# Kernel optimization log

Measured on AMD Instinct MI355X. Metric: run time of the kernel, lower is better.

## Reference

```python
import jax, jax.numpy as jnp
import numpy as np

B, S, E, H = 4, 2048, 1024, 16
D = E // H  # head_dim


def setup_inputs() -> dict:
    key = jax.random.key(0)
    ks = jax.random.split(key, 7)
    scale = 1.0 / np.sqrt(E)
    return {
        "query": jax.random.normal(ks[0], (B, S, E), dtype=jnp.float32),
        "key": jax.random.normal(ks[1], (B, S, E), dtype=jnp.float32),
        "value": jax.random.normal(ks[2], (B, S, E), dtype=jnp.float32),
        "Wq": jax.random.normal(ks[3], (E, E), dtype=jnp.float32) * scale,
        "Wk": jax.random.normal(ks[4], (E, E), dtype=jnp.float32) * scale,
        "Wv": jax.random.normal(ks[5], (E, E), dtype=jnp.float32) * scale,
        "Wo": jax.random.normal(ks[6], (E, E), dtype=jnp.float32) * scale,
    }


def reference(query, key, value, Wq, Wk, Wv, Wo):
    b, s, e = query.shape
    sm_scale = (e // H) ** -0.5
    # TTLinear: x @ W.T; reshape to [b, h, s, d]
    q = (query @ Wq.T).reshape(b, s, H, D).transpose(0, 2, 1, 3)
    k = (key @ Wk.T).reshape(b, s, H, D).transpose(0, 2, 1, 3)
    v = (value @ Wv.T).reshape(b, s, H, D).transpose(0, 2, 1, 3)
    scores = jnp.einsum("bhqd,bhkd->bhqk", q, k) * sm_scale  # [b,h,s,s]
    attn = jax.nn.softmax(scores, axis=-1)
    out = jnp.einsum("bhqk,bhkd->bhqd", attn, v)
    out = out.transpose(0, 2, 1, 3).reshape(b, s, e)
    # dropout is identity in eval mode
    return out @ Wo.T
```

## Files before the change

kernel.cpp:

```cpp
#include <hip/hip_runtime.h>
#include <hip/hip_bf16.h>

#define BB 4
#define SS 2048
#define EE 1024
#define HH 16
#define DD 64
#define MM (BB*SS)

using f16x8 = __attribute__((ext_vector_type(8))) _Float16;
using f16x4 = __attribute__((ext_vector_type(4))) _Float16;
using f32x4 = __attribute__((ext_vector_type(4))) float;
using f32x16 = __attribute__((ext_vector_type(16))) float;

typedef __attribute__((address_space(3))) void       as3_void;
typedef const __attribute__((address_space(1))) void as1_cvoid;

__device__ __forceinline__ void async16(void* lds, const void* g) {
    __builtin_amdgcn_global_load_lds((as1_cvoid*)g, (as3_void*)lds, 16, 0, 0);
}

__device__ __forceinline__ f16x8 cvt8(const float* src) {
    const float4 v0 = *(const float4*)src;
    const float4 v1 = *(const float4*)(src + 4);
    f16x8 h;
    h[0] = (_Float16)v0.x; h[1] = (_Float16)v0.y;
    h[2] = (_Float16)v0.z; h[3] = (_Float16)v0.w;
    h[4] = (_Float16)v1.x; h[5] = (_Float16)v1.y;
    h[6] = (_Float16)v1.z; h[7] = (_Float16)v1.w;
    return h;
}

__global__ __launch_bounds__(256) void cvt_all(const float* __restrict__ q,
                                               const float* __restrict__ k,
                                               const float* __restrict__ v,
                                               const float* __restrict__ w0,
                                               const float* __restrict__ w1,
                                               const float* __restrict__ w2,
                                               const float* __restrict__ w3,
                                               _Float16* __restrict__ dq,
                                               _Float16* __restrict__ dk,
                                               _Float16* __restrict__ dv,
                                               _Float16* __restrict__ wf,
                                               int aN8, int wN8) {
    int seg = blockIdx.y;
    int i = blockIdx.x * 256 + threadIdx.x;
    const float* s; _Float16* d; int n8;
    if (seg < 3) {
        s = seg == 0 ? q : seg == 1 ? k : v;
        d = seg == 0 ? dq : seg == 1 ? dk : dv;
        n8 = aN8;
    } else {
        int t = seg - 3;
        s = t == 0 ? w0 : t == 1 ? w1 : t == 2 ? w2 : w3;
        d = wf + (size_t)t * EE * EE;
        n8 = wN8;
    }
    if (i < n8) ((f16x8*)d)[i] = cvt8(s + (size_t)i * 8);
}

__device__ __forceinline__ void swizzle512(int fid, int& m0, int& n0) {
    int xcd  = fid & 7;
    int s    = fid >> 3;
    int band = xcd + 8 * (s >> 5);
    int w    = s & 31;
    m0 = (band * 4 + (w & 3)) * 128;
    n0 = (w >> 2) * 128;
}

__global__ __launch_bounds__(256) void gemm_qkv(const _Float16* __restrict__ A0,
                                                const _Float16* __restrict__ A1,
                                                const _Float16* __restrict__ A2,
                                                const _Float16* __restrict__ W,
                                                _Float16* __restrict__ Cb,
                                                int M, int N, int K) {
    constexpr int BM = 128, BN = 128, BK = 64;
    __shared__ alignas(16) _Float16 As[2][BM * 32];
    __shared__ alignas(16) _Float16 Bs[2][BN * 32];

    const int tid  = threadIdx.x;
    const int lane = tid & 63;
    const int wave = tid >> 6;
    const int wm   = (wave >> 1) * 64;
    const int wn   = (wave & 1) * 64;
    const int quad = lane >> 4;
    const int c    = lane & 15;
    int m0, n0;
    swizzle512(blockIdx.x, m0, n0);
    const int z = blockIdx.y;

    const _Float16* A  = z == 0 ? A0 : z == 1 ? A1 : A2;
    const _Float16* Bw = W + (size_t)z * EE * EE;
    _Float16* C = Cb + (size_t)z * MM * EE;
    const float osc = (z == 0) ? 0.18033688f : 1.0f;

    f32x4 acc[4][4] = {};

    for (int k0 = 0; k0 < K; k0 += BK) {
#pragma unroll
        for (int p = 0; p < 4; ++p) {
            int half = p >> 1;
            int remb = (p & 1) * 256 + wave * 64;
            int rem  = remb + lane;
            int row  = rem >> 2, kc = (rem & 3) * 8;
            async16(&As[half][remb * 8], A  + (size_t)(m0 + row) * K + k0 + half * 32 + kc);
            async16(&Bs[half][remb * 8], Bw + (size_t)(n0 + row) * K + k0 + half * 32 + kc);
        }
        __syncthreads();

#pragma unroll
        for (int ks = 0; ks < 2; ++ks) {
            f16x8 af[4], bf[4];
#pragma unroll
            for (int i = 0; i < 4; ++i)
                af[i] = *(const f16x8*)&As[ks][(wm + i * 16 + c) * 32 + quad * 8];
#pragma unroll
            for (int j = 0; j < 4; ++j)
                bf[j] = *(const f16x8*)&Bs[ks][(wn + j * 16 + c) * 32 + quad * 8];
#pragma unroll
            for (int i = 0; i < 4; ++i)
#pragma unroll
                for (int j = 0; j < 4; ++j)
                    acc[i][j] = __builtin_amdgcn_mfma_f32_16x16x32_f16(af[i], bf[j], acc[i][j], 0, 0, 0);
        }
        __syncthreads();
    }

    if (z == 2) {
#pragma unroll
        for (int i = 0; i < 4; ++i)
#pragma unroll
            for (int j = 0; j < 4; ++j) {
                int col  = n0 + wn + j * 16 + c;
                int rowb = m0 + wm + i * 16 + quad * 4;
                int bq = rowb >> 11, sI = rowb & 2047;
                f16x4 ov;
#pragma unroll
                for (int r = 0; r < 4; ++r) ov[r] = (_Float16)acc[i][j][r];
                *(f16x4*)&C[(((size_t)bq * HH + (col >> 6)) * DD + (col & 63)) * SS + sI] = ov;
            }
    } else {
#pragma unroll
        for (int i = 0; i < 4; ++i)
#pragma unroll
            for (int j = 0; j < 4; ++j)
#pragma unroll
                for (int r = 0; r < 4; ++r) {
                    int row = m0 + wm + i * 16 + quad * 4 + r;
                    int col = n0 + wn + j * 16 + c;
                    C[(size_t)row * N + col] = (_Float16)(acc[i][j][r] * osc);
                }
    }
}

__global__ __launch_bounds__(256) void gemm_wo(const _Float16* __restrict__ A,
                                               const _Float16* __restrict__ Bw,
                                               float* __restrict__ C,
                                               int M, int N, int K) {
    constexpr int BM = 128, BN = 128, BK = 64;
    __shared__ alignas(16) _Float16 As[2][BM * 32];
    __shared__ alignas(16) _Float16 Bs[2][BN * 32];

    const int tid  = threadIdx.x;
    const int lane = tid & 63;
    const int wave = tid >> 6;
    const int wm   = (wave >> 1) * 64;
    const int wn   = (wave & 1) * 64;
    const int quad = lane >> 4;
    const int c    = lane & 15;
    int m0, n0;
    swizzle512(blockIdx.x, m0, n0);

    f32x4 acc[4][4] = {};

    for (int k0 = 0; k0 < K; k0 += BK) {
#pragma unroll
        for (int p = 0; p < 4; ++p) {
            int half = p >> 1;
            int remb = (p & 1) * 256 + wave * 64;
            int rem  = remb + lane;
            int row  = rem >> 2, kc = (rem & 3) * 8;
            async16(&As[half][remb * 8], A  + (size_t)(m0 + row) * K + k0 + half * 32 + kc);
            async16(&Bs[half][remb * 8], Bw + (size_t)(n0 + row) * K + k0 + half * 32 + kc);
        }
        __syncthreads();

#pragma unroll
        for (int ks = 0; ks < 2; ++ks) {
            f16x8 af[4], bf[4];
#pragma unroll
            for (int i = 0; i < 4; ++i)
                af[i] = *(const f16x8*)&As[ks][(wm + i * 16 + c) * 32 + quad * 8];
#pragma unroll
            for (int j = 0; j < 4; ++j)
                bf[j] = *(const f16x8*)&Bs[ks][(wn + j * 16 + c) * 32 + quad * 8];
#pragma unroll
            for (int i = 0; i < 4; ++i)
#pragma unroll
                for (int j = 0; j < 4; ++j)
                    acc[i][j] = __builtin_amdgcn_mfma_f32_16x16x32_f16(af[i], bf[j], acc[i][j], 0, 0, 0);
        }
        __syncthreads();
    }

#pragma unroll
    for (int i = 0; i < 4; ++i)
#pragma unroll
        for (int j = 0; j < 4; ++j)
#pragma unroll
            for (int r = 0; r < 4; ++r) {
                int row = m0 + wm + i * 16 + quad * 4 + r;
                int col = n0 + wn + j * 16 + c;
                C[(size_t)row * N + col] = acc[i][j][r];
            }
}

__global__ __launch_bounds__(256, 4) void attn_kernel(const _Float16* __restrict__ Q,
                                                      const _Float16* __restrict__ K,
                                                      const _Float16* __restrict__ Vt,
                                                      _Float16* __restrict__ O) {
    constexpr int NT = SS / 64;
    __shared__ alignas(16) _Float16 Ks[2][8 * 512];
    __shared__ alignas(16) _Float16 Vs[2][8 * 512];

    const int tid  = threadIdx.x;
    const int lane = tid & 63;
    const int wave = tid >> 6;
    const int l31  = lane & 31;
    const int hl   = lane >> 5;
    const int bh   = blockIdx.x;
    const int b    = bh >> 4, h = bh & 15;
    const int q0   = blockIdx.y * 128;

    const _Float16* Qg  = Q  + (size_t)(b * SS + q0) * EE + h * DD;
    const _Float16* Kg  = K  + (size_t)(b * SS) * EE + h * DD;
    const _Float16* Vtg = Vt + (size_t)bh * DD * SS;

    f16x8 qf[4];
#pragma unroll
    for (int ks = 0; ks < 4; ++ks)
        qf[ks] = *(const f16x8*)(Qg + (size_t)(wave * 32 + l31) * EE + ks * 16 + hl * 8);

    const _Float16* kp[2];
    const _Float16* vp[2];
#pragma unroll
    for (int p = 0; p < 2; ++p) {
        int f = wave * 2 + p;
        int kvt = f >> 2, ksk = f & 3;
        kp[p] = Kg + (size_t)(kvt * 32 + l31) * EE + ksk * 16 + hl * 8;
        int ksv = f >> 1, dt = f & 1;
        vp[p] = Vtg + (size_t)(dt * 32 + l31) * SS + ksv * 16 + hl * 8;
    }

#pragma unroll
    for (int p = 0; p < 2; ++p) {
        int f = wave * 2 + p;
        async16(&Ks[0][f * 512], kp[p]);
        async16(&Vs[0][f * 512], vp[p]);
    }
    __syncthreads();

    float lsum = 0.f;
    f32x16 o0 = {}, o1 = {};

    for (int t = 0; t < NT; ++t) {
        const int buf = t & 1;

        if (t + 1 < NT) {
#pragma unroll
            for (int p = 0; p < 2; ++p) {
                int f = wave * 2 + p;
                kp[p] += 64 * EE;
                vp[p] += 64;
                async16(&Ks[buf ^ 1][f * 512], kp[p]);
                async16(&Vs[buf ^ 1][f * 512], vp[p]);
            }
        }

        f32x16 sa = {}, sb = {};
        __builtin_amdgcn_s_setprio(1);
#pragma unroll
        for (int ks = 0; ks < 4; ++ks) {
            f16x8 af = *(const f16x8*)&Ks[buf][ks * 512 + lane * 8];
            sa = __builtin_amdgcn_mfma_f32_32x32x16_f16(af, qf[ks], sa, 0, 0, 0);
        }
#pragma unroll
        for (int ks = 0; ks < 4; ++ks) {
            f16x8 af = *(const f16x8*)&Ks[buf][(4 + ks) * 512 + lane * 8];
            sb = __builtin_amdgcn_mfma_f32_32x32x16_f16(af, qf[ks], sb, 0, 0, 0);
        }
        __builtin_amdgcn_s_setprio(0);

        f16x8 pB[4];
#pragma unroll
        for (int kvt = 0; kvt < 2; ++kvt) {
            const f32x16& s = kvt ? sb : sa;
            float p[16];
#pragma unroll
            for (int r = 0; r < 16; ++r) {
                p[r] = __builtin_amdgcn_exp2f(s[r]);
                lsum += p[r];
            }
            int w[8];
#pragma unroll
            for (int i = 0; i < 8; ++i)
                w[i] = __builtin_bit_cast(int, __builtin_amdgcn_cvt_pkrtz(p[2 * i], p[2 * i + 1]));
            asm("v_permlane32_swap_b32 %0, %1" : "+v"(w[0]), "+v"(w[2]));
            asm("v_permlane32_swap_b32 %0, %1" : "+v"(w[1]), "+v"(w[3]));
            asm("v_permlane32_swap_b32 %0, %1" : "+v"(w[4]), "+v"(w[6]));
            asm("v_permlane32_swap_b32 %0, %1" : "+v"(w[5]), "+v"(w[7]));
            int4 lo; lo.x = w[0]; lo.y = w[1]; lo.z = w[2]; lo.w = w[3];
            int4 hi; hi.x = w[4]; hi.y = w[5]; hi.z = w[6]; hi.w = w[7];
            pB[kvt * 2 + 0] = __builtin_bit_cast(f16x8, lo);
            pB[kvt * 2 + 1] = __builtin_bit_cast(f16x8, hi);

            __builtin_amdgcn_s_setprio(1);
#pragma unroll
            for (int ks = kvt * 2; ks < kvt * 2 + 2; ++ks) {
                f16x8 v0 = *(const f16x8*)&Vs[buf][(ks * 2 + 0) * 512 + lane * 8];
                o0 = __builtin_amdgcn_mfma_f32_32x32x16_f16(v0, pB[ks], o0, 0, 0, 0);
                f16x8 v1 = *(const f16x8*)&Vs[buf][(ks * 2 + 1) * 512 + lane * 8];
                o1 = __builtin_amdgcn_mfma_f32_32x32x16_f16(v1, pB[ks], o1, 0, 0, 0);
            }
            __builtin_amdgcn_s_setprio(0);
        }

        __syncthreads();
    }

    float lt  = lsum + __shfl_xor(lsum, 32);
    float inv = 1.0f / lt;
    _Float16* Og = O + (size_t)(b * SS + q0 + wave * 32 + l31) * EE + h * DD;
#pragma unroll
    for (int dt = 0; dt < 2; ++dt)
#pragma unroll
        for (int g = 0; g < 4; ++g) {
            f16x4 ov;
#pragma unroll
            for (int r = 0; r < 4; ++r) {
                float val = (dt == 0) ? o0[g * 4 + r] : o1[g * 4 + r];
                ov[r] = (_Float16)(val * inv);
            }
            *(f16x4*)&Og[dt * 32 + g * 8 + hl * 4] = ov;
        }
}

extern "C" void kernel_launch(void* const* d_in, const int* in_sizes, int n_in,
                              void* d_out, int out_size, void* d_ws, size_t ws_size,
                              hipStream_t stream) {
    const float* query = (const float*)d_in[0];
    const float* key   = (const float*)d_in[1];
    const float* value = (const float*)d_in[2];
    const float* Wq    = (const float*)d_in[3];
    const float* Wk    = (const float*)d_in[4];
    const float* Wv    = (const float*)d_in[5];
    const float* Wo    = (const float*)d_in[6];
    float* out = (float*)d_out;

    const size_t NE = (size_t)MM * EE;
    const size_t NW = (size_t)EE * EE;
    _Float16* Qw   = (_Float16*)d_ws;
    _Float16* Kw   = Qw + NE;
    _Float16* Vw   = Kw + NE;
    _Float16* Wf   = Vw + NE;
    _Float16* Qact = Wf + 4 * NW;
    _Float16* Kact = (_Float16*)d_out;
    _Float16* Vact = Kact + NE;

    dim3 blk(256);
    const int wN8 = (int)(NW / 8), aN8 = (int)(NE / 8);

    cvt_all<<<dim3(aN8 / 256, 7), blk, 0, stream>>>(query, key, value, Wq, Wk, Wv, Wo,
                                                    Qact, Kact, Vact, Wf, aN8, wN8);

    gemm_qkv<<<dim3(512, 3), blk, 0, stream>>>(Qact, Kact, Vact, Wf, Qw, MM, EE, EE);

    attn_kernel<<<dim3(BB * HH, SS / 128), blk, 0, stream>>>(Qw, Kw, Vw, Qact);

    gemm_wo<<<dim3(512), blk, 0, stream>>>(Qact, Wf + 3 * NW, out, MM, EE, EE);
}
```

Before: 340.0 us.

## Stage V-transpose epilogue through LDS and interleave score MFMAs

The V projection epilogue now writes its tile into LDS with an XOR swizzle, then reads it back transposed so each lane stores contiguous 16-byte chunks along the sequence dimension, replacing the scattered 8-byte strided global stores. In the attention kernel, the two score MFMA chains are interleaved to expose independent work, and the row-sum accumulation is split into four partial sums to shorten the dependency chain. This costs an extra barrier and LDS round trip in the GEMM epilogue and slightly changes the order of the floating-point sums.

```diff
diff --git a/kernel.cpp b/kernel.cpp
--- a/kernel.cpp
+++ b/kernel.cpp
@@ -127,18 +127,34 @@
     }
 
     if (z == 2) {
+        _Float16* tb = (wave < 2) ? ((_Float16*)As) + wave * 4096
+                                  : ((_Float16*)Bs) + (wave - 2) * 4096;
 #pragma unroll
         for (int i = 0; i < 4; ++i)
 #pragma unroll
             for (int j = 0; j < 4; ++j) {
-                int col  = n0 + wn + j * 16 + c;
-                int rowb = m0 + wm + i * 16 + quad * 4;
-                int bq = rowb >> 11, sI = rowb & 2047;
+                int dl = j * 16 + c;
+                int sl = i * 16 + quad * 4;
                 f16x4 ov;
 #pragma unroll
                 for (int r = 0; r < 4; ++r) ov[r] = (_Float16)acc[i][j][r];
-                *(f16x4*)&C[(((size_t)bq * HH + (col >> 6)) * DD + (col & 63)) * SS + sI] = ov;
-            }
+                *(f16x4*)&tb[dl * 64 + (sl ^ ((dl & 7) << 3))] = ov;
+            }
+        __syncthreads();
+        const int colbase = n0 + wn;
+        const int h  = colbase >> 6;
+        const int rowb = m0 + wm;
+        const int bq = rowb >> 11;
+        const int s_base = rowb & 2047;
+        const int dr0 = lane >> 3;
+        const int sc  = (lane & 7) * 8;
+        _Float16* Vtb = C + (((size_t)bq * HH + h) * DD) * SS;
+#pragma unroll
+        for (int dd = 0; dd < 8; ++dd) {
+            int d = dd * 8 + dr0;
+            f16x8 vv = *(const f16x8*)&tb[d * 64 + (sc ^ ((d & 7) << 3))];
+            *(f16x8*)&Vtb[(size_t)d * SS + s_base + sc] = vv;
+        }
     } else {
 #pragma unroll
         for (int i = 0; i < 4; ++i)
@@ -260,7 +276,7 @@
     }
     __syncthreads();
 
-    float lsum = 0.f;
+    float ls[4] = {0.f, 0.f, 0.f, 0.f};
     f32x16 o0 = {}, o1 = {};
 
     for (int t = 0; t < NT; ++t) {
@@ -281,13 +297,10 @@
         __builtin_amdgcn_s_setprio(1);
 #pragma unroll
         for (int ks = 0; ks < 4; ++ks) {
-            f16x8 af = *(const f16x8*)&Ks[buf][ks * 512 + lane * 8];
-            sa = __builtin_amdgcn_mfma_f32_32x32x16_f16(af, qf[ks], sa, 0, 0, 0);
-        }
-#pragma unroll
-        for (int ks = 0; ks < 4; ++ks) {
-            f16x8 af = *(const f16x8*)&Ks[buf][(4 + ks) * 512 + lane * 8];
-            sb = __builtin_amdgcn_mfma_f32_32x32x16_f16(af, qf[ks], sb, 0, 0, 0);
+            f16x8 a0 = *(const f16x8*)&Ks[buf][ks * 512 + lane * 8];
+            f16x8 a1 = *(const f16x8*)&Ks[buf][(4 + ks) * 512 + lane * 8];
+            sa = __builtin_amdgcn_mfma_f32_32x32x16_f16(a0, qf[ks], sa, 0, 0, 0);
+            sb = __builtin_amdgcn_mfma_f32_32x32x16_f16(a1, qf[ks], sb, 0, 0, 0);
         }
         __builtin_amdgcn_s_setprio(0);
 
@@ -299,7 +312,7 @@
 #pragma unroll
             for (int r = 0; r < 16; ++r) {
                 p[r] = __builtin_amdgcn_exp2f(s[r]);
-                lsum += p[r];
+                ls[r & 3] += p[r];
             }
             int w[8];
 #pragma unroll
@@ -328,6 +341,7 @@
         __syncthreads();
     }
 
+    float lsum = (ls[0] + ls[1]) + (ls[2] + ls[3]);
     float lt  = lsum + __shfl_xor(lsum, 32);
     float inv = 1.0f / lt;
     _Float16* Og = O + (size_t)(b * SS + q0 + wave * 32 + l31) * EE + h * DD;
```

New measurement: 337.6 us. No clear change (-0.7%).
